# Optimization experiments

Measured on AMD Instinct MI355X. Metric: run time of the kernel, lower is better.

## Reference

```python
import jax, jax.numpy as jnp
import numpy as np
from jax import lax

C = 64          # grid_channels
RGB = 3         # rgb_channels
D = 128         # conditioning_dim
NUM_CLASSES = 1000
HIDDEN = 256    # hypernet hidden
NUM_STEPS = 32
TOT1 = C * C * 9


def setup_inputs() -> dict:
    key = jax.random.key(0)
    ks = jax.random.split(key, 20)
    s = 0.02
    B, H, W = 32, 64, 64
    return {
        "class_labels": jax.random.randint(ks[0], (B,), 0, NUM_CLASSES),
        "initial_grid": jax.random.normal(ks[1], (B, C, H, W), jnp.float32) * 0.1,
        "emb": jax.random.normal(ks[2], (NUM_CLASSES, D), jnp.float32) * s,
        "hw1": jax.random.normal(ks[3], (D, HIDDEN), jnp.float32) * s,
        "hb1": jnp.zeros((HIDDEN,), jnp.float32),
        "hw2": jax.random.normal(ks[4], (HIDDEN, HIDDEN), jnp.float32) * s,
        "hb2": jnp.zeros((HIDDEN,), jnp.float32),
        "hw3": jax.random.normal(ks[5], (HIDDEN, 2 * TOT1), jnp.float32) * s,
        "hb3": jnp.zeros((2 * TOT1,), jnp.float32),
        "f1w1": jax.random.normal(ks[6], (D, D), jnp.float32) * s,
        "f1b1": jnp.zeros((D,), jnp.float32),
        "f1w2": jax.random.normal(ks[7], (D, 2 * C), jnp.float32) * s,
        "f1b2": jnp.concatenate([jnp.ones((C,), jnp.float32), jnp.zeros((C,), jnp.float32)]),
        "f2w1": jax.random.normal(ks[8], (D, D), jnp.float32) * s,
        "f2b1": jnp.zeros((D,), jnp.float32),
        "f2w2": jax.random.normal(ks[9], (D, 2 * C), jnp.float32) * s,
        "f2b2": jnp.concatenate([jnp.ones((C,), jnp.float32), jnp.zeros((C,), jnp.float32)]),
        "blend": jnp.float32(0.5),
    }


def _conv_circ_one(x, w):
    # x: [C,H,W], w: [Cout,Cin,3,3]; circular pad then VALID conv == padding=1 circular
    xp = jnp.pad(x, ((0, 0), (1, 1), (1, 1)), mode='wrap')
    return lax.conv_general_dilated(xp[None], w, (1, 1), 'VALID')[0]

_bconv = jax.vmap(_conv_circ_one)  # per-sample dynamic weights over batch


def _film_params(cond, w1, b1, w2, b2):
    p = jax.nn.relu(cond @ w1 + b1) @ w2 + b2  # [B, 2C]
    return p[:, :C, None, None], p[:, C:, None, None]


def reference(class_labels, initial_grid, emb, hw1, hb1, hw2, hb2, hw3, hb3,
              f1w1, f1b1, f1w2, f1b2, f2w1, f2b1, f2w2, f2b2, blend):
    cond = emb[class_labels]                       # [B, D]
    h = jax.nn.relu(cond @ hw1 + hb1)
    h = jax.nn.relu(h @ hw2 + hb2)
    weights = h @ hw3 + hb3                        # [B, 2*C*C*9]
    B = cond.shape[0]
    w1 = weights[:, :TOT1].reshape(B, C, C, 3, 3)
    w2 = weights[:, TOT1:].reshape(B, C, C, 3, 3)
    g1, be1 = _film_params(cond, f1w1, f1b1, f1w2, f1b2)
    g2, be2 = _film_params(cond, f2w1, f2b1, f2w2, f2b2)
    blend_s = jax.nn.sigmoid(blend)

    def step(grid, _):
        u = jax.nn.relu(g1 * _bconv(grid, w1) + be1)
        u = jax.nn.relu(g2 * _bconv(u, w2) + be2)
        grid = (1 - blend_s) * grid + blend_s * u
        rgb = jax.nn.sigmoid(grid[:, :RGB])
        return grid, rgb

    _, traj = lax.scan(step, initial_grid, None, length=NUM_STEPS)  # [T,B,3,H,W]
    return traj[-1], traj
```

## Files before the change

kernel.cpp:

```cpp
#include <hip/hip_runtime.h>


typedef __attribute__((ext_vector_type(8))) short short8;
typedef __attribute__((ext_vector_type(4))) float f32x4;
typedef __attribute__((ext_vector_type(8))) unsigned short us8;

__device__ __forceinline__ unsigned short f2bf(float f) {
  unsigned int u = __builtin_bit_cast(unsigned int, f);
  u = (u + 0x7FFFu + ((u >> 16) & 1u)) >> 16;
  return (unsigned short)u;
}
__device__ __forceinline__ float bf2f(unsigned short h) {
  unsigned int u = ((unsigned int)h) << 16;
  return __builtin_bit_cast(float, u);
}

__device__ __forceinline__ void gl_lds16(const void* g, void* l) {
  __builtin_amdgcn_global_load_lds((const __attribute__((address_space(1))) void*)g,
                                   (__attribute__((address_space(3))) void*)l, 16, 0, 0);
}

__global__ void hyper_kernel(const int* __restrict__ labels, const float* __restrict__ emb,
                             const float* __restrict__ hw1, const float* __restrict__ hb1,
                             const float* __restrict__ hw2, const float* __restrict__ hb2,
                             float* __restrict__ h2T) {
  __shared__ float cond[128];
  __shared__ float h1[256];
  const int s = blockIdx.x, j = threadIdx.x;
  if (j < 128) cond[j] = emb[(size_t)labels[s] * 128 + j];
  __syncthreads();
  float a = hb1[j];
  for (int k = 0; k < 128; ++k) a += cond[k] * hw1[k * 256 + j];
  h1[j] = fmaxf(a, 0.f);
  __syncthreads();
  float a2 = hb2[j];
  for (int k = 0; k < 256; ++k) a2 += h1[k] * hw2[k * 256 + j];
  h2T[j * 32 + s] = fmaxf(a2, 0.f);
}

__global__ void film_kernel(const int* __restrict__ labels, const float* __restrict__ emb,
                            const float* __restrict__ f1w1, const float* __restrict__ f1b1,
                            const float* __restrict__ f1w2, const float* __restrict__ f1b2,
                            const float* __restrict__ f2w1, const float* __restrict__ f2b1,
                            const float* __restrict__ f2w2, const float* __restrict__ f2b2,
                            float* __restrict__ film) {
  __shared__ float cond[128];
  __shared__ float hid[128];
  const int s = blockIdx.x, which = blockIdx.y, j = threadIdx.x;
  const float* W1 = which ? f2w1 : f1w1;
  const float* B1 = which ? f2b1 : f1b1;
  const float* W2 = which ? f2w2 : f1w2;
  const float* B2 = which ? f2b2 : f1b2;
  cond[j] = emb[(size_t)labels[s] * 128 + j];
  __syncthreads();
  float a = B1[j];
  for (int k = 0; k < 128; ++k) a += cond[k] * W1[k * 128 + j];
  hid[j] = fmaxf(a, 0.f);
  __syncthreads();
  float p = B2[j];
  for (int k = 0; k < 128; ++k) p += hid[k] * W2[k * 128 + j];
  film[(size_t)((which * 2 + (j >> 6)) * 32 + s) * 64 + (j & 63)] = p;
}

__launch_bounds__(256)
__global__ void wgen_kernel(const float* __restrict__ h2T, const float* __restrict__ hw3,
                            const float* __restrict__ hb3, unsigned short* __restrict__ W) {
  __shared__ float h2l[8192];
  const int t = threadIdx.x;
  for (int i = t; i < 8192; i += 256) h2l[i] = h2T[i];
  __syncthreads();
  const int j0 = blockIdx.x * 512 + t * 2;
  float a0[32], a1[32];
  #pragma unroll
  for (int i = 0; i < 32; ++i) { a0[i] = 0.f; a1[i] = 0.f; }
  #pragma unroll 4
  for (int k = 0; k < 256; ++k) {
    const float2 wv = *(const float2*)&hw3[(size_t)k * 73728 + j0];
    const float4* h4 = (const float4*)&h2l[k * 32];
    #pragma unroll
    for (int q = 0; q < 8; ++q) {
      const float4 h = h4[q];
      a0[q*4+0] += h.x * wv.x; a1[q*4+0] += h.x * wv.y;
      a0[q*4+1] += h.y * wv.x; a1[q*4+1] += h.y * wv.y;
      a0[q*4+2] += h.z * wv.x; a1[q*4+2] += h.z * wv.y;
      a0[q*4+3] += h.w * wv.x; a1[q*4+3] += h.w * wv.y;
    }
  }
  #pragma unroll
  for (int jj = 0; jj < 2; ++jj) {
    const int j  = j0 + jj;
    const float bias = hb3[j];
    const int cv = j / 36864;
    const int r  = j - cv * 36864;
    const int co = r / 576;
    const int r2 = r - co * 576;
    const int ci = r2 / 9;
    const int tap = r2 - ci * 9;
    const int sw = (co * 64 + ci) ^ ((co & 7) << 3);
    #pragma unroll
    for (int s2 = 0; s2 < 32; ++s2) {
      const float v = (jj ? a1[s2] : a0[s2]) + bias;
      W[(size_t)((s2 * 2 + cv) * 9 + tap) * 4096 + sw] = f2bf(v);
    }
  }
}

__global__ void init_kernel(const float* __restrict__ gin, unsigned short* __restrict__ g0) {
  __shared__ float lds[64][65];
  const int b = blockIdx.x >> 6, y = blockIdx.x & 63;
  const int t = threadIdx.x;
  {
    const int ci = t >> 2, xq = t & 3;
    const float* base = gin + (size_t)((b * 64 + ci) * 64 + y) * 64;
    #pragma unroll
    for (int q = 0; q < 4; ++q) {
      const int x0 = (xq + q * 4) * 4;
      const float4 v = *(const float4*)(base + x0);
      lds[ci][x0+0] = v.x; lds[ci][x0+1] = v.y; lds[ci][x0+2] = v.z; lds[ci][x0+3] = v.w;
    }
  }
  __syncthreads();
  const int x = t >> 2, cq = t & 3, ci0 = cq * 16;
  us8 lo, hi;
  #pragma unroll
  for (int i = 0; i < 8; ++i) lo[i] = f2bf(lds[ci0 + i][x]);
  #pragma unroll
  for (int i = 0; i < 8; ++i) hi[i] = f2bf(lds[ci0 + 8 + i][x]);
  char* dbase = (char*)(g0 + (size_t)(b * 64 + y) * 4096);
  const int o = x * 128 + ci0 * 2, sw = (x & 7) << 4;
  *(us8*)(dbase + (o ^ sw)) = lo;
  *(us8*)(dbase + ((o + 16) ^ sw)) = hi;
}

template<int WHICH>
__launch_bounds__(256, 2)
__global__ void conv_kernel(const unsigned short* __restrict__ Wall,
                            const unsigned short* __restrict__ src,
                            unsigned short* __restrict__ dst,
                            const unsigned short* __restrict__ gold,
                            const float* __restrict__ film,
                            const float* __restrict__ blendp,
                            float* __restrict__ out, int t) {
  __shared__ unsigned short in_lds[6 * 4096];
  __shared__ unsigned short w_lds[2][4096];
  const int tid  = threadIdx.x;
  const int wid  = tid >> 6;
  const int lane = tid & 63;
  const int l15  = lane & 15;
  const int lhi  = lane >> 4;
  const int s    = blockIdx.x >> 4;
  const int y0   = (blockIdx.x & 15) * 4;

  const unsigned short* srcs = src + (size_t)s * 262144;
  const unsigned short* Wb   = Wall + (size_t)((s * 2 + WHICH) * 9) * 4096;

  #pragma unroll
  for (int q = 0; q < 12; ++q) {
    const int idx = q * 4 + wid;
    const int row = idx >> 3, ch = idx & 7;
    const int ry  = (y0 + row + 63) & 63;
    gl_lds16(srcs + ry * 4096 + ch * 512 + lane * 8, &in_lds[row * 4096 + ch * 512]);
  }
  #pragma unroll
  for (int q = 0; q < 2; ++q) {
    const int idx = q * 4 + wid;
    gl_lds16(Wb + idx * 512 + lane * 8, &w_lds[0][idx * 512]);
  }
  asm volatile("s_waitcnt vmcnt(0)" ::: "memory");
  __syncthreads();

  f32x4 acc[4][4];
  #pragma unroll
  for (int m = 0; m < 4; ++m)
    #pragma unroll
    for (int n = 0; n < 4; ++n)
      #pragma unroll
      for (int j = 0; j < 4; ++j) acc[m][n][j] = 0.f;

  #pragma unroll
  for (int tap = 0; tap < 9; ++tap) {
    const int cur = tap & 1;
    if (tap < 8) {
      #pragma unroll
      for (int q = 0; q < 2; ++q) {
        const int idx = q * 4 + wid;
        gl_lds16(Wb + (tap + 1) * 4096 + idx * 512 + lane * 8, &w_lds[cur ^ 1][idx * 512]);
      }
    }
    const int ky = tap / 3, kx = tap % 3;
    short8 af[4][2], bfr[4][2];
    #pragma unroll
    for (int m = 0; m < 4; ++m) {
      const int co = m * 16 + l15;
      #pragma unroll
      for (int kk = 0; kk < 2; ++kk) {
        const int off = (co * 128 + (kk * 32 + lhi * 8) * 2) ^ ((co & 7) << 4);
        af[m][kk] = *(const short8*)((const char*)&w_lds[cur][0] + off);
      }
    }
    const int r = wid + ky;
    #pragma unroll
    for (int n = 0; n < 4; ++n) {
      const int xs = (n * 16 + l15 + kx + 63) & 63;
      #pragma unroll
      for (int kk = 0; kk < 2; ++kk) {
        const int off = (r * 8192 + xs * 128 + (kk * 32 + lhi * 8) * 2) ^ ((xs & 7) << 4);
        bfr[n][kk] = *(const short8*)((const char*)in_lds + off);
      }
    }
    #pragma unroll
    for (int kk = 0; kk < 2; ++kk)
      #pragma unroll
      for (int m = 0; m < 4; ++m)
        #pragma unroll
        for (int n = 0; n < 4; ++n)
          acc[m][n] = __builtin_amdgcn_mfma_f32_16x16x32_bf16(af[m][kk], bfr[n][kk], acc[m][n], 0, 0, 0);
    if (tap < 8) {
      asm volatile("s_waitcnt vmcnt(0)" ::: "memory");
      __syncthreads();
    }
  }

  const int y = y0 + wid;
  const float* fg = film + WHICH * 2 * 2048;
  const float* fb = fg + 2048;
  float bs = 0.f, obs = 0.f;
  if (WHICH == 1) { bs = 1.f / (1.f + expf(-blendp[0])); obs = 1.f - bs; }
  unsigned short* drow = dst + (size_t)s * 262144 + y * 4096;
  const unsigned short* grow = (WHICH == 1) ? (gold + (size_t)s * 262144 + y * 4096) : (const unsigned short*)nullptr;

  #pragma unroll
  for (int m = 0; m < 4; ++m) {
    const int co0 = m * 16 + lhi * 4;
    const float4 g  = *(const float4*)&fg[s * 64 + co0];
    const float4 be = *(const float4*)&fb[s * 64 + co0];
    #pragma unroll
    for (int n = 0; n < 4; ++n) {
      const int x = n * 16 + l15;
      const int off = (x * 128 + co0 * 2) ^ ((x & 7) << 4);
      const f32x4 v = acc[m][n];
      const float u0 = fmaxf(g.x * v[0] + be.x, 0.f);
      const float u1 = fmaxf(g.y * v[1] + be.y, 0.f);
      const float u2 = fmaxf(g.z * v[2] + be.z, 0.f);
      const float u3 = fmaxf(g.w * v[3] + be.w, 0.f);
      if (WHICH == 0) {
        ushort4 pk; pk.x = f2bf(u0); pk.y = f2bf(u1); pk.z = f2bf(u2); pk.w = f2bf(u3);
        *(ushort4*)((char*)drow + off) = pk;
      } else {
        const ushort4 od = *(const ushort4*)((const char*)grow + off);
        const float g0 = obs * bf2f(od.x) + bs * u0;
        const float g1 = obs * bf2f(od.y) + bs * u1;
        const float g2 = obs * bf2f(od.z) + bs * u2;
        const float g3 = obs * bf2f(od.w) + bs * u3;
        ushort4 pk; pk.x = f2bf(g0); pk.y = f2bf(g1); pk.z = f2bf(g2); pk.w = f2bf(g3);
        *(ushort4*)((char*)drow + off) = pk;
        if (co0 == 0) {
          const float r0 = 1.f / (1.f + expf(-g0));
          const float r1 = 1.f / (1.f + expf(-g1));
          const float r2 = 1.f / (1.f + expf(-g2));
          float* ob = out + 393216 + (size_t)((t * 32 + s) * 3) * 4096 + y * 64 + x;
          ob[0] = r0; ob[4096] = r1; ob[8192] = r2;
          if (t == 31) {
            float* o2 = out + (size_t)(s * 3) * 4096 + y * 64 + x;
            o2[0] = r0; o2[4096] = r1; o2[8192] = r2;
          }
        }
      }
    }
  }
}

extern "C" void kernel_launch(void* const* d_in, const int* in_sizes, int n_in,
                              void* d_out, int out_size, void* d_ws, size_t ws_size,
                              hipStream_t stream) {
  (void)in_sizes; (void)n_in; (void)out_size; (void)ws_size;
  const int*   labels = (const int*)d_in[0];
  const float* gin    = (const float*)d_in[1];
  const float* emb    = (const float*)d_in[2];
  const float* hw1    = (const float*)d_in[3];
  const float* hb1    = (const float*)d_in[4];
  const float* hw2    = (const float*)d_in[5];
  const float* hb2    = (const float*)d_in[6];
  const float* hw3    = (const float*)d_in[7];
  const float* hb3    = (const float*)d_in[8];
  const float* f1w1   = (const float*)d_in[9];
  const float* f1b1   = (const float*)d_in[10];
  const float* f1w2   = (const float*)d_in[11];
  const float* f1b2   = (const float*)d_in[12];
  const float* f2w1   = (const float*)d_in[13];
  const float* f2b1   = (const float*)d_in[14];
  const float* f2w2   = (const float*)d_in[15];
  const float* f2b2   = (const float*)d_in[16];
  const float* blend  = (const float*)d_in[17];
  float* out = (float*)d_out;

  char* ws = (char*)d_ws;
  unsigned short* grid0 = (unsigned short*)(ws + (size_t)0);
  unsigned short* grid1 = (unsigned short*)(ws + (size_t)16777216);
  unsigned short* ubuf  = (unsigned short*)(ws + (size_t)33554432);
  unsigned short* Wbuf  = (unsigned short*)(ws + (size_t)50331648);
  float* h2T  = (float*)(ws + (size_t)55050240);
  float* film = (float*)(ws + (size_t)55083008);

  hyper_kernel<<<32, 256, 0, stream>>>(labels, emb, hw1, hb1, hw2, hb2, h2T);
  film_kernel<<<dim3(32, 2), 128, 0, stream>>>(labels, emb, f1w1, f1b1, f1w2, f1b2,
                                               f2w1, f2b1, f2w2, f2b2, film);
  wgen_kernel<<<144, 256, 0, stream>>>(h2T, hw3, hb3, Wbuf);
  init_kernel<<<2048, 256, 0, stream>>>(gin, grid0);

  for (int t = 0; t < 32; ++t) {
    unsigned short* gi = (t & 1) ? grid1 : grid0;
    unsigned short* go = (t & 1) ? grid0 : grid1;
    conv_kernel<0><<<512, 256, 0, stream>>>(Wbuf, gi, ubuf, nullptr, film, nullptr, nullptr, t);
    conv_kernel<1><<<512, 256, 0, stream>>>(Wbuf, ubuf, go, gi, film, blend, out, t);
  }
}
```

Before: 1.395 ms.

## Enlarge conv tiles to 8 rows with all taps' weights resident in LDS

The conv kernel now runs 512-thread blocks covering 8 output rows, loading the 10-row input halo and all 9 weight taps into LDS up front. This removes the per-tap double-buffered weight loads and the per-tap barriers, and cuts halo re-reads. The cost is much more LDS per block (about 152KB), which may allow only one block per CU, and a 256-block grid that may leave CUs idle. Separately, wgen is re-parallelized over more blocks, with each thread computing 8 samples for one output column instead of 32 samples for two.

Measured after the change: 1.430 ms. 2.5% more time.

```diff
diff --git a/kernel.cpp b/kernel.cpp
--- a/kernel.cpp
+++ b/kernel.cpp
@@ -69,39 +69,32 @@
   const int t = threadIdx.x;
   for (int i = t; i < 8192; i += 256) h2l[i] = h2T[i];
   __syncthreads();
-  const int j0 = blockIdx.x * 512 + t * 2;
-  float a0[32], a1[32];
-  #pragma unroll
-  for (int i = 0; i < 32; ++i) { a0[i] = 0.f; a1[i] = 0.f; }
+  const int j  = blockIdx.x * 64 + (t & 63);
+  const int sg = t >> 6;
+  float acc[8];
+  #pragma unroll
+  for (int i = 0; i < 8; ++i) acc[i] = 0.f;
+  const float* hp = &h2l[sg * 8];
   #pragma unroll 4
   for (int k = 0; k < 256; ++k) {
-    const float2 wv = *(const float2*)&hw3[(size_t)k * 73728 + j0];
-    const float4* h4 = (const float4*)&h2l[k * 32];
-    #pragma unroll
-    for (int q = 0; q < 8; ++q) {
-      const float4 h = h4[q];
-      a0[q*4+0] += h.x * wv.x; a1[q*4+0] += h.x * wv.y;
-      a0[q*4+1] += h.y * wv.x; a1[q*4+1] += h.y * wv.y;
-      a0[q*4+2] += h.z * wv.x; a1[q*4+2] += h.z * wv.y;
-      a0[q*4+3] += h.w * wv.x; a1[q*4+3] += h.w * wv.y;
-    }
-  }
-  #pragma unroll
-  for (int jj = 0; jj < 2; ++jj) {
-    const int j  = j0 + jj;
-    const float bias = hb3[j];
-    const int cv = j / 36864;
-    const int r  = j - cv * 36864;
-    const int co = r / 576;
-    const int r2 = r - co * 576;
-    const int ci = r2 / 9;
-    const int tap = r2 - ci * 9;
-    const int sw = (co * 64 + ci) ^ ((co & 7) << 3);
-    #pragma unroll
-    for (int s2 = 0; s2 < 32; ++s2) {
-      const float v = (jj ? a1[s2] : a0[s2]) + bias;
-      W[(size_t)((s2 * 2 + cv) * 9 + tap) * 4096 + sw] = f2bf(v);
-    }
+    const float w = hw3[(size_t)k * 73728 + j];
+    const float4 hA = *(const float4*)(hp + k * 32);
+    const float4 hB = *(const float4*)(hp + k * 32 + 4);
+    acc[0] += hA.x * w; acc[1] += hA.y * w; acc[2] += hA.z * w; acc[3] += hA.w * w;
+    acc[4] += hB.x * w; acc[5] += hB.y * w; acc[6] += hB.z * w; acc[7] += hB.w * w;
+  }
+  const float bias = hb3[j];
+  const int cv = j / 36864;
+  const int r  = j - cv * 36864;
+  const int co = r / 576;
+  const int r2 = r - co * 576;
+  const int ci = r2 / 9;
+  const int tap = r2 - ci * 9;
+  const int sw = (co * 64 + ci) ^ ((co & 7) << 3);
+  #pragma unroll
+  for (int i = 0; i < 8; ++i) {
+    const int s2 = sg * 8 + i;
+    W[(size_t)((s2 * 2 + cv) * 9 + tap) * 4096 + sw] = f2bf(acc[i] + bias);
   }
 }
 
@@ -133,7 +126,7 @@
 }
 
 template<int WHICH>
-__launch_bounds__(256, 2)
+__launch_bounds__(512, 2)
 __global__ void conv_kernel(const unsigned short* __restrict__ Wall,
                             const unsigned short* __restrict__ src,
                             unsigned short* __restrict__ dst,
@@ -141,30 +134,30 @@
                             const float* __restrict__ film,
                             const float* __restrict__ blendp,
                             float* __restrict__ out, int t) {
-  __shared__ unsigned short in_lds[6 * 4096];
-  __shared__ unsigned short w_lds[2][4096];
+  __shared__ unsigned short in_lds[10 * 4096];
+  __shared__ unsigned short w_lds[9 * 4096];
   const int tid  = threadIdx.x;
   const int wid  = tid >> 6;
   const int lane = tid & 63;
   const int l15  = lane & 15;
   const int lhi  = lane >> 4;
-  const int s    = blockIdx.x >> 4;
-  const int y0   = (blockIdx.x & 15) * 4;
+  const int s    = blockIdx.x >> 3;
+  const int y0   = (blockIdx.x & 7) * 8;
 
   const unsigned short* srcs = src + (size_t)s * 262144;
   const unsigned short* Wb   = Wall + (size_t)((s * 2 + WHICH) * 9) * 4096;
 
   #pragma unroll
-  for (int q = 0; q < 12; ++q) {
-    const int idx = q * 4 + wid;
-    const int row = idx >> 3, ch = idx & 7;
-    const int ry  = (y0 + row + 63) & 63;
-    gl_lds16(srcs + ry * 4096 + ch * 512 + lane * 8, &in_lds[row * 4096 + ch * 512]);
-  }
-  #pragma unroll
-  for (int q = 0; q < 2; ++q) {
-    const int idx = q * 4 + wid;
-    gl_lds16(Wb + idx * 512 + lane * 8, &w_lds[0][idx * 512]);
+  for (int q = 0; q < 10; ++q) {
+    const int c   = q * 8 + wid;
+    const int row = c >> 3, part = c & 7;
+    const int gy  = (y0 + row + 63) & 63;
+    gl_lds16(srcs + gy * 4096 + part * 512 + lane * 8, &in_lds[row * 4096 + part * 512]);
+  }
+  #pragma unroll
+  for (int q = 0; q < 9; ++q) {
+    const int c = q * 8 + wid;
+    gl_lds16(Wb + c * 512 + lane * 8, &w_lds[c * 512]);
   }
   asm volatile("s_waitcnt vmcnt(0)" ::: "memory");
   __syncthreads();
@@ -179,14 +172,6 @@
 
   #pragma unroll
   for (int tap = 0; tap < 9; ++tap) {
-    const int cur = tap & 1;
-    if (tap < 8) {
-      #pragma unroll
-      for (int q = 0; q < 2; ++q) {
-        const int idx = q * 4 + wid;
-        gl_lds16(Wb + (tap + 1) * 4096 + idx * 512 + lane * 8, &w_lds[cur ^ 1][idx * 512]);
-      }
-    }
     const int ky = tap / 3, kx = tap % 3;
     short8 af[4][2], bfr[4][2];
     #pragma unroll
@@ -194,8 +179,8 @@
       const int co = m * 16 + l15;
       #pragma unroll
       for (int kk = 0; kk < 2; ++kk) {
-        const int off = (co * 128 + (kk * 32 + lhi * 8) * 2) ^ ((co & 7) << 4);
-        af[m][kk] = *(const short8*)((const char*)&w_lds[cur][0] + off);
+        const int off = tap * 8192 + ((co * 128 + kk * 64 + lhi * 16) ^ ((co & 7) << 4));
+        af[m][kk] = *(const short8*)((const char*)w_lds + off);
       }
     }
     const int r = wid + ky;
@@ -204,7 +189,7 @@
       const int xs = (n * 16 + l15 + kx + 63) & 63;
       #pragma unroll
       for (int kk = 0; kk < 2; ++kk) {
-        const int off = (r * 8192 + xs * 128 + (kk * 32 + lhi * 8) * 2) ^ ((xs & 7) << 4);
+        const int off = r * 8192 + ((xs * 128 + kk * 64 + lhi * 16) ^ ((xs & 7) << 4));
         bfr[n][kk] = *(const short8*)((const char*)in_lds + off);
       }
     }
@@ -215,10 +200,6 @@
         #pragma unroll
         for (int n = 0; n < 4; ++n)
           acc[m][n] = __builtin_amdgcn_mfma_f32_16x16x32_bf16(af[m][kk], bfr[n][kk], acc[m][n], 0, 0, 0);
-    if (tap < 8) {
-      asm volatile("s_waitcnt vmcnt(0)" ::: "memory");
-      __syncthreads();
-    }
   }
 
   const int y = y0 + wid;
@@ -305,13 +286,13 @@
   hyper_kernel<<<32, 256, 0, stream>>>(labels, emb, hw1, hb1, hw2, hb2, h2T);
   film_kernel<<<dim3(32, 2), 128, 0, stream>>>(labels, emb, f1w1, f1b1, f1w2, f1b2,
                                                f2w1, f2b1, f2w2, f2b2, film);
-  wgen_kernel<<<144, 256, 0, stream>>>(h2T, hw3, hb3, Wbuf);
+  wgen_kernel<<<1152, 256, 0, stream>>>(h2T, hw3, hb3, Wbuf);
   init_kernel<<<2048, 256, 0, stream>>>(gin, grid0);
 
   for (int t = 0; t < 32; ++t) {
     unsigned short* gi = (t & 1) ? grid1 : grid0;
     unsigned short* go = (t & 1) ? grid0 : grid1;
-    conv_kernel<0><<<512, 256, 0, stream>>>(Wbuf, gi, ubuf, nullptr, film, nullptr, nullptr, t);
-    conv_kernel<1><<<512, 256, 0, stream>>>(Wbuf, ubuf, go, gi, film, blend, out, t);
-  }
-}
+    conv_kernel<0><<<256, 512, 0, stream>>>(Wbuf, gi, ubuf, nullptr, film, nullptr, nullptr, t);
+    conv_kernel<1><<<256, 512, 0, stream>>>(Wbuf, ubuf, go, gi, film, blend, out, t);
+  }
+}
```
